# Kernel optimization log

Measured on AMD Instinct MI355X. Metric: run time of the kernel, lower is better.

The kernel has to match this reference:

```python
import jax, jax.numpy as jnp
import numpy as np

B, T, D, H, FF, TB = 4, 512, 768, 12, 3072, 64
DK = D // H
E = float(np.e)
NEG = -1e9  # stand-in for float('-inf') masked_fill; rows always have valid entries


def layer_norm(x, g, b, eps=1e-5):
    m = jnp.mean(x, axis=-1, keepdims=True)
    v = jnp.mean((x - m) ** 2, axis=-1, keepdims=True)
    return (x - m) * jax.lax.rsqrt(v + eps) * g + b


def setup_inputs() -> dict:
    key = jax.random.key(0)
    ks = jax.random.split(key, 20)
    s = 0.02
    w = lambda k, shape: jax.random.normal(k, shape, jnp.float32) * s
    return {
        "x": jax.random.normal(ks[0], (B, T, D), jnp.float32),
        "batch_temporal_mat": jax.random.uniform(ks[1], (B, T, T), jnp.float32, 0.0, 100.0),
        "padding_masks": jnp.ones((B, 1, T, T), jnp.int32),
        # attention linears (stored (in,out): y = x @ W + b, equals torch x @ W_t.T + b)
        "wq": w(ks[2], (D, D)), "bq": w(ks[3], (D,)),
        "wk": w(ks[4], (D, D)), "bk": w(ks[5], (D,)),
        "wv": w(ks[6], (D, D)), "bv": w(ks[7], (D,)),
        "wp": w(ks[8], (D, D)), "bp": w(ks[9], (D,)),
        # temporal-bias MLP: Linear(1,TB) -> leaky_relu(0.2) -> Linear(TB,1)
        "tb1_w": w(ks[10], (1, TB)), "tb1_b": w(ks[11], (TB,)),
        "tb2_w": w(ks[12], (TB, 1)), "tb2_b": w(ks[13], (1,)),
        # FFN
        "fc1_w": w(ks[14], (D, FF)), "fc1_b": w(ks[15], (FF,)),
        "fc2_w": w(ks[16], (FF, D)), "fc2_b": w(ks[17], (D,)),
        # layernorms
        "ln1_g": jnp.ones((D,), jnp.float32), "ln1_b": jnp.zeros((D,), jnp.float32),
        "ln2_g": jnp.ones((D,), jnp.float32), "ln2_b": jnp.zeros((D,), jnp.float32),
    }


def _block(x, batch_temporal_mat, padding_masks,
           wq, bq, wk, bk, wv, bv, wp, bp,
           tb1_w, tb1_b, tb2_w, tb2_b,
           fc1_w, fc1_b, fc2_w, fc2_b,
           ln1_g, ln1_b, ln2_g, ln2_b):
    # pre-LN attention sublayer
    h = layer_norm(x, ln1_g, ln1_b)
    q = (h @ wq + bq).reshape(B, T, H, DK).transpose(0, 2, 1, 3)  # (B,H,T,DK)
    k = (h @ wk + bk).reshape(B, T, H, DK).transpose(0, 2, 1, 3)
    v = (h @ wv + bv).reshape(B, T, H, DK).transpose(0, 2, 1, 3)
    scores = jnp.einsum('bhid,bhjd->bhij', q, k) * (DK ** -0.5)  # (B,H,T,T)

    # temporal bias: 1/log(e + dt), then per-(i,j) MLP with leaky_relu(0.2)
    tm = 1.0 / jnp.log(E + batch_temporal_mat)                    # (B,T,T)
    hb = jax.nn.leaky_relu(tm[..., None] @ tb1_w + tb1_b, 0.2)    # (B,T,T,TB)
    bias = (hb @ tb2_w + tb2_b)[..., 0]                           # (B,T,T)
    scores = scores + bias[:, None]

    # padding mask then causal (future) mask with CLS row 0 fully visible
    scores = jnp.where(padding_masks == 0, NEG, scores)
    causal = jnp.triu(jnp.ones((T, T), bool), 1).at[0, :].set(False)
    scores = jnp.where(causal, NEG, scores)

    p = jax.nn.softmax(scores, axis=-1)
    out = jnp.einsum('bhij,bhjd->bhid', p, v).transpose(0, 2, 1, 3).reshape(B, T, D)
    out = out @ wp + bp
    x = x + out

    # pre-LN FFN sublayer (exact GELU as in nn.GELU default)
    h2 = layer_norm(x, ln2_g, ln2_b)
    m = jax.nn.gelu(h2 @ fc1_w + fc1_b, approximate=False) @ fc2_w + fc2_b
    return x + m


def reference(x, batch_temporal_mat, padding_masks,
              wq, bq, wk, bk, wv, bv, wp, bp,
              tb1_w, tb1_b, tb2_w, tb2_b,
              fc1_w, fc1_b, fc2_w, fc2_b,
              ln1_g, ln1_b, ln2_g, ln2_b):
    return _block(x, batch_temporal_mat, padding_masks,
                  wq, bq, wk, bk, wv, bv, wp, bp,
                  tb1_w, tb1_b, tb2_w, tb2_b,
                  fc1_w, fc1_b, fc2_w, fc2_b,
                  ln1_g, ln1_b, ln2_g, ln2_b)
```

## Files before the change

### kernel.cpp

```cpp
#include <hip/hip_runtime.h>
#include <hip/hip_bf16.h>
#include <math.h>

#define B_ 4
#define T_ 512
#define D_ 768
#define H_ 12
#define FF_ 3072
#define DK_ 64
#define NTOK (B_*T_)
#define NEGV -1e9f

typedef unsigned short u16;
typedef __bf16 bfx8 __attribute__((ext_vector_type(8)));
typedef float f32x4 __attribute__((ext_vector_type(4)));
typedef u16 u16x8 __attribute__((ext_vector_type(8)));

__device__ __forceinline__ u16 f2bf(float f) {
  union { float f; unsigned u; } v; v.f = f;
  unsigned r = (v.u + 0x7FFFu + ((v.u >> 16) & 1u)) >> 16;
  return (u16)r;
}

__device__ __forceinline__ void glds16(const u16* g, u16* l) {
  __builtin_amdgcn_global_load_lds((const __attribute__((address_space(1))) void*)g,
                                   (__attribute__((address_space(3))) void*)l, 16, 0, 0);
}

__global__ __launch_bounds__(256) void prep_kernel(
    const float* __restrict__ x,
    const float* __restrict__ wq, const float* __restrict__ wk,
    const float* __restrict__ wv, const float* __restrict__ wp,
    const float* __restrict__ fc1, const float* __restrict__ fc2,
    u16* wqT, u16* wkT, u16* wvT, u16* wpT, u16* fc1T, u16* fc2T,
    const float* __restrict__ ln1g, const float* __restrict__ ln1b, u16* __restrict__ hbuf,
    const float* __restrict__ bp, float* __restrict__ x1,
    const float* __restrict__ tmat, const int* __restrict__ pad,
    const float* __restrict__ tb1w, const float* __restrict__ tb1b,
    const float* __restrict__ tb2w, const float* __restrict__ tb2b,
    float* __restrict__ biasM)
{
  const int bid = blockIdx.x;
  const int tid = threadIdx.x;
  if (bid < 6912) {
    __shared__ float tile[32][33];
    const float* in; u16* outp; int K, N, local;
    if (bid < 2304) {
      int m = bid / 576; local = bid % 576; K = 768; N = 768;
      in   = m == 0 ? wq  : (m == 1 ? wk  : (m == 2 ? wv  : wp));
      outp = m == 0 ? wqT : (m == 1 ? wkT : (m == 2 ? wvT : wpT));
    } else if (bid < 4608) {
      local = bid - 2304; K = 768; N = 3072; in = fc1; outp = fc1T;
    } else {
      local = bid - 4608; K = 3072; N = 768; in = fc2; outp = fc2T;
    }
    const int nt = N / 32;
    const int n0 = (local % nt) * 32, k0 = (local / nt) * 32;
    const int tx = tid & 31, ty = tid >> 5;
    #pragma unroll
    for (int i = 0; i < 4; ++i) {
      int r = ty + i * 8;
      tile[r][tx] = in[(size_t)(k0 + r) * N + n0 + tx];
    }
    __syncthreads();
    #pragma unroll
    for (int i = 0; i < 4; ++i) {
      int r = ty + i * 8;
      outp[(size_t)(n0 + r) * K + k0 + tx] = f2bf(tile[tx][r]);
    }
  } else if (bid < 8960) {
    const int row = bid - 6912;
    const float* xr = x + (size_t)row * D_;
    float v0 = xr[tid], v1 = xr[tid + 256], v2 = xr[tid + 512];
    float s = v0 + v1 + v2;
    float sq = v0 * v0 + v1 * v1 + v2 * v2;
    #pragma unroll
    for (int o = 32; o > 0; o >>= 1) { s += __shfl_down(s, o); sq += __shfl_down(sq, o); }
    __shared__ float ss[4], s2[4];
    int w = tid >> 6;
    if ((tid & 63) == 0) { ss[w] = s; s2[w] = sq; }
    __syncthreads();
    s = ss[0] + ss[1] + ss[2] + ss[3];
    sq = s2[0] + s2[1] + s2[2] + s2[3];
    float mean = s * (1.0f / 768.0f);
    float inv = rsqrtf(sq * (1.0f / 768.0f) - mean * mean + 1e-5f);
    u16* orow = hbuf + (size_t)row * D_;
    float* x1r = x1 + (size_t)row * D_;
    orow[tid]       = f2bf((v0 - mean) * inv * ln1g[tid]       + ln1b[tid]);
    orow[tid + 256] = f2bf((v1 - mean) * inv * ln1g[tid + 256] + ln1b[tid + 256]);
    orow[tid + 512] = f2bf((v2 - mean) * inv * ln1g[tid + 512] + ln1b[tid + 512]);
    x1r[tid]       = v0 + bp[tid];
    x1r[tid + 256] = v1 + bp[tid + 256];
    x1r[tid + 512] = v2 + bp[tid + 512];
  } else {
    __shared__ float sw1[64], sb1[64], sw2[64];
    if (tid < 64) {
      sw1[tid] = tb1w[tid];
      sb1[tid] = tb1b[tid];
      sw2[tid] = tb2w[tid];
    }
    __syncthreads();
    size_t idx = (size_t)(bid - 8960) * 256 + tid;
    float tm = 1.0f / __logf(2.718281828459045f + tmat[idx]);
    float acc = tb2b[0];
    #pragma unroll
    for (int t = 0; t < 64; ++t) {
      float u = fmaf(tm, sw1[t], sb1[t]);
      u = u > 0.0f ? u : 0.2f * u;
      acc = fmaf(u, sw2[t], acc);
    }
    biasM[idx] = (pad[idx] == 0) ? NEGV : acc;
  }
}

__device__ __forceinline__ void gemm_tile_p2(
    const u16* __restrict__ A, const u16* __restrict__ BT,
    int K, int nk, int m0, int n0, int k0,
    u16* As, u16* Bs, f32x4 acc[4][4])
{
  const int tid = threadIdx.x;
  const int w = tid >> 6, lane = tid & 63;
  const int lr = lane & 15, lk = (lane >> 4) * 8;
  const int wm = (w >> 1) * 64, wn = (w & 1) * 64;
  const int c0 = w * 64 + lane, c1 = 256 + c0;
  const int r0 = c0 >> 2, o0 = (c0 & 3) * 8;
  const int r1 = c1 >> 2, o1 = (c1 & 3) * 8;
  const u16* gA0 = A  + (size_t)(m0 + r0) * K + k0 + o0;
  const u16* gA1 = A  + (size_t)(m0 + r1) * K + k0 + o1;
  const u16* gB0 = BT + (size_t)(n0 + r0) * K + k0 + o0;
  const u16* gB1 = BT + (size_t)(n0 + r1) * K + k0 + o1;
  u16* la0 = As + w * 512;
  u16* la1 = As + 2048 + w * 512;
  u16* lb0 = Bs + w * 512;
  u16* lb1 = Bs + 2048 + w * 512;
#define ISSUE_TILE(kk, b) do { \
    glds16(gA0 + (size_t)(kk) * 32, la0 + (b) * 4096); \
    glds16(gA1 + (size_t)(kk) * 32, la1 + (b) * 4096); \
    glds16(gB0 + (size_t)(kk) * 32, lb0 + (b) * 4096); \
    glds16(gB1 + (size_t)(kk) * 32, lb1 + (b) * 4096); } while (0)
  ISSUE_TILE(0, 0);
  if (nk > 1) ISSUE_TILE(1, 1);
  int cb = 0;
  for (int kt = 0; kt < nk; ++kt) {
    if (kt < nk - 2) asm volatile("s_waitcnt vmcnt(4)" ::: "memory");
    else             asm volatile("s_waitcnt vmcnt(0)" ::: "memory");
    __builtin_amdgcn_sched_barrier(0);
    __builtin_amdgcn_s_barrier();
    __builtin_amdgcn_sched_barrier(0);
    const u16* Asc = As + cb * 4096;
    const u16* Bsc = Bs + cb * 4096;
    bfx8 af[4], bfr[4];
    #pragma unroll
    for (int t = 0; t < 4; ++t) {
      af[t]  = *(const bfx8*)&Asc[(wm + t * 16 + lr) * 32 + lk];
      bfr[t] = *(const bfx8*)&Bsc[(wn + t * 16 + lr) * 32 + lk];
    }
    #pragma unroll
    for (int rt = 0; rt < 4; ++rt)
      #pragma unroll
      for (int ct = 0; ct < 4; ++ct)
        acc[rt][ct] = __builtin_amdgcn_mfma_f32_16x16x32_bf16(af[rt], bfr[ct], acc[rt][ct], 0, 0, 0);
    if (kt + 2 < nk) {
      int nb = cb + 2; if (nb >= 3) nb -= 3;
      ISSUE_TILE(kt + 2, nb);
    }
    cb = cb + 1; if (cb >= 3) cb = 0;
  }
#undef ISSUE_TILE
}

__global__ __launch_bounds__(256) void gemm_qkv(
    const u16* __restrict__ A,
    const u16* __restrict__ wqT, const u16* __restrict__ wkT, const u16* __restrict__ wvT,
    const float* __restrict__ bq, const float* __restrict__ bk, const float* __restrict__ bv,
    u16* __restrict__ qo, u16* __restrict__ ko, u16* __restrict__ vo)
{
  __shared__ u16 As[3 * 128 * 32];
  __shared__ u16 Bs[3 * 128 * 32];
  const int z = blockIdx.z;
  const u16* BT = z == 0 ? wqT : (z == 1 ? wkT : wvT);
  const float* bias = z == 0 ? bq : (z == 1 ? bk : bv);
  u16* outp = z == 0 ? qo : (z == 1 ? ko : vo);
  const float scale = z == 0 ? 0.125f : 1.0f;
  const int m0 = blockIdx.y * 128, n0 = blockIdx.x * 128;
  f32x4 acc[4][4];
  #pragma unroll
  for (int a = 0; a < 4; ++a)
    #pragma unroll
    for (int bb = 0; bb < 4; ++bb) acc[a][bb] = (f32x4){0.f, 0.f, 0.f, 0.f};
  gemm_tile_p2(A, BT, D_, D_ / 32, m0, n0, 0, As, Bs, acc);
  const int tid = threadIdx.x;
  const int w = tid >> 6, lane = tid & 63;
  const int lr = lane & 15;
  const int wm = (w >> 1) * 64, wn = (w & 1) * 64;
  #pragma unroll
  for (int rt = 0; rt < 4; ++rt)
    #pragma unroll
    for (int ct = 0; ct < 4; ++ct)
      #pragma unroll
      for (int r = 0; r < 4; ++r) {
        int m = m0 + wm + rt * 16 + (lane >> 4) * 4 + r;
        int n = n0 + wn + ct * 16 + lr;
        float val = (acc[rt][ct][r] + bias[n]) * scale;
        int b = m >> 9, t = m & 511, hh = n >> 6, d = n & 63;
        if (z < 2) outp[(((size_t)b * H_ + hh) * T_ + t) * DK_ + d] = f2bf(val);
        else       outp[(((size_t)b * H_ + hh) * DK_ + d) * T_ + t] = f2bf(val);
      }
}

__global__ __launch_bounds__(256) void gemm_atomic(
    const u16* __restrict__ A, const u16* __restrict__ BT,
    float* __restrict__ dst, int M, int N, int K, int Ksplit)
{
  __shared__ u16 As[3 * 128 * 32];
  __shared__ u16 Bs[3 * 128 * 32];
  const int m0 = blockIdx.y * 128, n0 = blockIdx.x * 128;
  const int kz = blockIdx.z;
  f32x4 acc[4][4];
  #pragma unroll
  for (int a = 0; a < 4; ++a)
    #pragma unroll
    for (int bb = 0; bb < 4; ++bb) acc[a][bb] = (f32x4){0.f, 0.f, 0.f, 0.f};
  gemm_tile_p2(A, BT, K, Ksplit / 32, m0, n0, kz * Ksplit, As, Bs, acc);
  const int tid = threadIdx.x;
  const int w = tid >> 6, lane = tid & 63;
  const int lr = lane & 15;
  const int wm = (w >> 1) * 64, wn = (w & 1) * 64;
  #pragma unroll
  for (int rt = 0; rt < 4; ++rt)
    #pragma unroll
    for (int ct = 0; ct < 4; ++ct)
      #pragma unroll
      for (int r = 0; r < 4; ++r) {
        int m = m0 + wm + rt * 16 + (lane >> 4) * 4 + r;
        int n = n0 + wn + ct * 16 + lr;
        atomicAdd(&dst[(size_t)m * N + n], acc[rt][ct][r]);
      }
}

__global__ __launch_bounds__(256) void gemm_gelu(
    const u16* __restrict__ A, const u16* __restrict__ BT,
    const float* __restrict__ bias, u16* __restrict__ outp, int M, int N, int K)
{
  __shared__ u16 As[3 * 128 * 32];
  __shared__ u16 Bs[3 * 128 * 32];
  const int m0 = blockIdx.y * 128, n0 = blockIdx.x * 128;
  f32x4 acc[4][4];
  #pragma unroll
  for (int a = 0; a < 4; ++a)
    #pragma unroll
    for (int bb = 0; bb < 4; ++bb) acc[a][bb] = (f32x4){0.f, 0.f, 0.f, 0.f};
  gemm_tile_p2(A, BT, K, K / 32, m0, n0, 0, As, Bs, acc);
  const int tid = threadIdx.x;
  const int w = tid >> 6, lane = tid & 63;
  const int lr = lane & 15;
  const int wm = (w >> 1) * 64, wn = (w & 1) * 64;
  #pragma unroll
  for (int rt = 0; rt < 4; ++rt)
    #pragma unroll
    for (int ct = 0; ct < 4; ++ct)
      #pragma unroll
      for (int r = 0; r < 4; ++r) {
        int m = m0 + wm + rt * 16 + (lane >> 4) * 4 + r;
        int n = n0 + wn + ct * 16 + lr;
        float val = acc[rt][ct][r] + bias[n];
        float gl = 0.5f * val * (1.0f + erff(val * 0.7071067811865475f));
        outp[(size_t)m * N + n] = f2bf(gl);
      }
}

__global__ __launch_bounds__(256) void ln2_kernel(
    const float* __restrict__ x1, const float* __restrict__ g, const float* __restrict__ bta,
    const float* __restrict__ fc2b, u16* __restrict__ h2, float* __restrict__ outInit)
{
  const int row = blockIdx.x;
  const int tid = threadIdx.x;
  const size_t base = (size_t)row * D_;
  float v[3];
  float s = 0.f, sq = 0.f;
  #pragma unroll
  for (int i = 0; i < 3; ++i) {
    int c = tid + i * 256;
    float val = x1[base + c];
    v[i] = val;
    s += val; sq += val * val;
  }
  #pragma unroll
  for (int o = 32; o > 0; o >>= 1) { s += __shfl_down(s, o); sq += __shfl_down(sq, o); }
  __shared__ float ss[4], s2[4];
  int w = tid >> 6;
  if ((tid & 63) == 0) { ss[w] = s; s2[w] = sq; }
  __syncthreads();
  s = ss[0] + ss[1] + ss[2] + ss[3];
  sq = s2[0] + s2[1] + s2[2] + s2[3];
  float mean = s * (1.0f / 768.0f);
  float inv = rsqrtf(sq * (1.0f / 768.0f) - mean * mean + 1e-5f);
  #pragma unroll
  for (int i = 0; i < 3; ++i) {
    int c = tid + i * 256;
    h2[base + c] = f2bf((v[i] - mean) * inv * g[c] + bta[c]);
    outInit[base + c] = v[i] + fc2b[c];
  }
}

__global__ __launch_bounds__(256) void attn_kernel(
    const u16* __restrict__ q, const u16* __restrict__ k, const u16* __restrict__ vT,
    const float* __restrict__ biasM, u16* __restrict__ ao)
{
  __shared__ u16 P[32 * 512];
  __shared__ float pmax[128], psum[128];
  const int tid = threadIdx.x;
  const int w = tid >> 6, lane = tid & 63;
  const int lr = lane & 15, hi = lane >> 4, lk = hi * 8;

  const int bid = blockIdx.x;
  const int xcd = bid & 7, idx = bid >> 3;
  const int bh = xcd * 6 + (idx >> 4);
  const int i0 = (idx & 15) * 32;
  const int b = bh / H_, h = bh % H_;
  const int tmax = (i0 == 0) ? 31 : ((i0 >> 4) + 1);
  const int nks  = (i0 == 0) ? 16 : ((i0 >> 5) + 1);

  bfx8 qf[2][2];
  #pragma unroll
  for (int g = 0; g < 2; ++g)
    #pragma unroll
    for (int ks = 0; ks < 2; ++ks)
      qf[g][ks] = *(const bfx8*)(q + ((size_t)bh * T_ + i0 + g * 16 + lr) * DK_ + ks * 32 + lk);
  f32x4 acc[8][2];
  float mx[2][4];
  #pragma unroll
  for (int g = 0; g < 2; ++g)
    #pragma unroll
    for (int r = 0; r < 4; ++r) mx[g][r] = -3.4e38f;
  #pragma unroll
  for (int ct = 0; ct < 8; ++ct) {
    const int t = ct * 4 + w;
    if (t > tmax) continue;
    const int j0 = t * 16;
    bfx8 kf0 = *(const bfx8*)(k + ((size_t)bh * T_ + j0 + lr) * DK_ + lk);
    bfx8 kf1 = *(const bfx8*)(k + ((size_t)bh * T_ + j0 + lr) * DK_ + 32 + lk);
    const int j = j0 + lr;
    #pragma unroll
    for (int g = 0; g < 2; ++g) {
      f32x4 a0 = (f32x4){0.f, 0.f, 0.f, 0.f};
      a0 = __builtin_amdgcn_mfma_f32_16x16x32_bf16(qf[g][0], kf0, a0, 0, 0, 0);
      a0 = __builtin_amdgcn_mfma_f32_16x16x32_bf16(qf[g][1], kf1, a0, 0, 0, 0);
      #pragma unroll
      for (int r = 0; r < 4; ++r) {
        int i = i0 + g * 16 + hi * 4 + r;
        float s = a0[r] + biasM[((size_t)b * T_ + i) * T_ + j];
        if (j > i && i != 0) s = NEGV;
        a0[r] = s;
        mx[g][r] = fmaxf(mx[g][r], s);
      }
      acc[ct][g] = a0;
    }
  }
  #pragma unroll
  for (int o = 1; o < 16; o <<= 1)
    #pragma unroll
    for (int g = 0; g < 2; ++g)
      #pragma unroll
      for (int r = 0; r < 4; ++r) mx[g][r] = fmaxf(mx[g][r], __shfl_xor(mx[g][r], o));
  if (lr == 0) {
    #pragma unroll
    for (int g = 0; g < 2; ++g)
      #pragma unroll
      for (int r = 0; r < 4; ++r) pmax[w * 32 + g * 16 + hi * 4 + r] = mx[g][r];
  }
  __syncthreads();

  float M2[2][4], sm[2][4];
  #pragma unroll
  for (int g = 0; g < 2; ++g)
    #pragma unroll
    for (int r = 0; r < 4; ++r) {
      int row = g * 16 + hi * 4 + r;
      M2[g][r] = fmaxf(fmaxf(pmax[row], pmax[32 + row]), fmaxf(pmax[64 + row], pmax[96 + row]));
      sm[g][r] = 0.f;
    }
  char* Pb = (char*)P;
  #pragma unroll
  for (int ct = 0; ct < 8; ++ct) {
    const int t = ct * 4 + w;
    if (t > tmax) continue;
    const int col = t * 16 + lr;
    #pragma unroll
    for (int g = 0; g < 2; ++g)
      #pragma unroll
      for (int r = 0; r < 4; ++r) {
        float pexp = __expf(acc[ct][g][r] - M2[g][r]);
        sm[g][r] += pexp;
        int row = g * 16 + hi * 4 + r;
        int byte = (row * 1024 + col * 2) ^ ((row & 7) << 4);
        *(u16*)(Pb + byte) = f2bf(pexp);
      }
  }
  #pragma unroll
  for (int o = 1; o < 16; o <<= 1)
    #pragma unroll
    for (int g = 0; g < 2; ++g)
      #pragma unroll
      for (int r = 0; r < 4; ++r) sm[g][r] += __shfl_xor(sm[g][r], o);
  if (lr == 0) {
    #pragma unroll
    for (int g = 0; g < 2; ++g)
      #pragma unroll
      for (int r = 0; r < 4; ++r) psum[w * 32 + g * 16 + hi * 4 + r] = sm[g][r];
  }
  __syncthreads();

  float rinv[2][4];
  #pragma unroll
  for (int g = 0; g < 2; ++g)
    #pragma unroll
    for (int r = 0; r < 4; ++r) {
      int row = g * 16 + hi * 4 + r;
      rinv[g][r] = 1.0f / (psum[row] + psum[32 + row] + psum[64 + row] + psum[96 + row]);
    }

  {
    const int n0 = w * 16;
    f32x4 oa0 = (f32x4){0.f, 0.f, 0.f, 0.f};
    f32x4 oa1 = (f32x4){0.f, 0.f, 0.f, 0.f};
    for (int ks = 0; ks < nks; ++ks) {
      bfx8 vf = *(const bfx8*)(vT + ((size_t)bh * DK_ + n0 + lr) * T_ + ks * 32 + lk);
      int byte0 = (lr * 1024 + (ks * 32 + lk) * 2) ^ ((lr & 7) << 4);
      int byte1 = ((16 + lr) * 1024 + (ks * 32 + lk) * 2) ^ ((lr & 7) << 4);
      bfx8 pa0 = *(const bfx8*)(Pb + byte0);
      bfx8 pa1 = *(const bfx8*)(Pb + byte1);
      oa0 = __builtin_amdgcn_mfma_f32_16x16x32_bf16(pa0, vf, oa0, 0, 0, 0);
      oa1 = __builtin_amdgcn_mfma_f32_16x16x32_bf16(pa1, vf, oa1, 0, 0, 0);
    }
    #pragma unroll
    for (int r = 0; r < 4; ++r) {
      int i = i0 + hi * 4 + r;
      ao[((size_t)b * T_ + i) * D_ + h * DK_ + n0 + lr] = f2bf(oa0[r] * rinv[0][r]);
    }
    #pragma unroll
    for (int r = 0; r < 4; ++r) {
      int i = i0 + 16 + hi * 4 + r;
      ao[((size_t)b * T_ + i) * D_ + h * DK_ + n0 + lr] = f2bf(oa1[r] * rinv[1][r]);
    }
  }
}

extern "C" void kernel_launch(void* const* d_in, const int* in_sizes, int n_in,
                              void* d_out, int out_size, void* d_ws, size_t ws_size,
                              hipStream_t stream) {
  (void)in_sizes; (void)n_in; (void)out_size; (void)ws_size;
  const float* x    = (const float*)d_in[0];
  const float* tmat = (const float*)d_in[1];
  const int*   pad  = (const int*)d_in[2];
  const float* wq = (const float*)d_in[3];  const float* bq = (const float*)d_in[4];
  const float* wk = (const float*)d_in[5];  const float* bk = (const float*)d_in[6];
  const float* wv = (const float*)d_in[7];  const float* bv = (const float*)d_in[8];
  const float* wp = (const float*)d_in[9];  const float* bp = (const float*)d_in[10];
  const float* tb1w = (const float*)d_in[11]; const float* tb1b = (const float*)d_in[12];
  const float* tb2w = (const float*)d_in[13]; const float* tb2b = (const float*)d_in[14];
  const float* fc1w = (const float*)d_in[15]; const float* fc1b = (const float*)d_in[16];
  const float* fc2w = (const float*)d_in[17]; const float* fc2b = (const float*)d_in[18];
  const float* ln1g = (const float*)d_in[19]; const float* ln1b = (const float*)d_in[20];
  const float* ln2g = (const float*)d_in[21]; const float* ln2b = (const float*)d_in[22];
  float* out = (float*)d_out;

  char* p = (char*)d_ws;
  u16* wqT  = (u16*)p; p += (size_t)768 * 768 * 2;
  u16* wkT  = (u16*)p; p += (size_t)768 * 768 * 2;
  u16* wvT  = (u16*)p; p += (size_t)768 * 768 * 2;
  u16* wpT  = (u16*)p; p += (size_t)768 * 768 * 2;
  u16* fc1T = (u16*)p; p += (size_t)768 * 3072 * 2;
  u16* fc2T = (u16*)p; p += (size_t)3072 * 768 * 2;
  float* x1 = (float*)p; p += (size_t)NTOK * D_ * 4;
  u16* gbuf = (u16*)p; p += (size_t)NTOK * FF_ * 2;
  u16* hbuf = (u16*)p; p += (size_t)NTOK * D_ * 2;
  u16* qb   = (u16*)p; p += (size_t)NTOK * D_ * 2;
  u16* kb   = (u16*)p; p += (size_t)NTOK * D_ * 2;
  u16* vTb  = (u16*)p; p += (size_t)NTOK * D_ * 2;
  float* biasM = (float*)p; p += (size_t)B_ * T_ * T_ * 4;
  u16* ao   = (u16*)p; p += (size_t)NTOK * D_ * 2;
  u16* h2   = (u16*)p; p += (size_t)NTOK * D_ * 2;

  prep_kernel<<<13056, 256, 0, stream>>>(x, wq, wk, wv, wp, fc1w, fc2w,
                                         wqT, wkT, wvT, wpT, fc1T, fc2T,
                                         ln1g, ln1b, hbuf, bp, x1,
                                         tmat, pad, tb1w, tb1b, tb2w, tb2b, biasM);

  gemm_qkv<<<dim3(6, 16, 3), 256, 0, stream>>>(hbuf, wqT, wkT, wvT, bq, bk, bv, qb, kb, vTb);
  attn_kernel<<<768, 256, 0, stream>>>(qb, kb, vTb, biasM, ao);

  gemm_atomic<<<dim3(6, 16, 2), 256, 0, stream>>>(ao, wpT, x1, NTOK, 768, 768, 384);
  ln2_kernel<<<NTOK, 256, 0, stream>>>(x1, ln2g, ln2b, fc2b, h2, out);

  gemm_gelu<<<dim3(24, 16), 256, 0, stream>>>(h2, fc1T, fc1b, gbuf, NTOK, FF_, 768);

  gemm_atomic<<<dim3(6, 16, 4), 256, 0, stream>>>(gbuf, fc2T, out, NTOK, 768, 3072, 768);
}
```

Before: 148.5 us.

## Replace atomic split-K with bf16 partials, XCD-aware tile mapping, and MFMA prio hints

Split-K GEMMs now write bf16 partial slabs instead of float atomics. Separate reduce kernels sum the partials together with the residual and biases, so the x1 and out initialisation moves out of prep and ln2. Grid indices are remapped so neighbouring M tiles share an XCD for L2 reuse, and the next tile load is issued before the MFMAs in the GEMM loop. Attention sets s_setprio around the MFMAs and splits the score epilogue from them, and the weight transpose stores vectorised u16x4. In exchange, the bf16 partials lose precision, the workspace grows by eight slabs, and there are extra partial writes and reads.

```diff
diff --git a/kernel.cpp b/kernel.cpp
--- a/kernel.cpp
+++ b/kernel.cpp
@@ -15,11 +15,16 @@
 typedef __bf16 bfx8 __attribute__((ext_vector_type(8)));
 typedef float f32x4 __attribute__((ext_vector_type(4)));
 typedef u16 u16x8 __attribute__((ext_vector_type(8)));
+typedef u16 u16x4 __attribute__((ext_vector_type(4)));
 
 __device__ __forceinline__ u16 f2bf(float f) {
   union { float f; unsigned u; } v; v.f = f;
   unsigned r = (v.u + 0x7FFFu + ((v.u >> 16) & 1u)) >> 16;
   return (u16)r;
+}
+
+__device__ __forceinline__ float bf2f(u16 u) {
+  union { unsigned u; float f; } c; c.u = (unsigned)u << 16; return c.f;
 }
 
 __device__ __forceinline__ void glds16(const u16* g, u16* l) {
@@ -34,7 +39,6 @@
     const float* __restrict__ fc1, const float* __restrict__ fc2,
     u16* wqT, u16* wkT, u16* wvT, u16* wpT, u16* fc1T, u16* fc2T,
     const float* __restrict__ ln1g, const float* __restrict__ ln1b, u16* __restrict__ hbuf,
-    const float* __restrict__ bp, float* __restrict__ x1,
     const float* __restrict__ tmat, const int* __restrict__ pad,
     const float* __restrict__ tb1w, const float* __restrict__ tb1b,
     const float* __restrict__ tb2w, const float* __restrict__ tb2b,
@@ -63,11 +67,12 @@
       tile[r][tx] = in[(size_t)(k0 + r) * N + n0 + tx];
     }
     __syncthreads();
-    #pragma unroll
-    for (int i = 0; i < 4; ++i) {
-      int r = ty + i * 8;
-      outp[(size_t)(n0 + r) * K + k0 + tx] = f2bf(tile[tx][r]);
-    }
+    const int nloc = tid >> 3;
+    const int k4   = (tid & 7) * 4;
+    u16x4 vv;
+    #pragma unroll
+    for (int jj = 0; jj < 4; ++jj) vv[jj] = f2bf(tile[k4 + jj][nloc]);
+    *(u16x4*)&outp[(size_t)(n0 + nloc) * K + k0 + k4] = vv;
   } else if (bid < 8960) {
     const int row = bid - 6912;
     const float* xr = x + (size_t)row * D_;
@@ -85,13 +90,9 @@
     float mean = s * (1.0f / 768.0f);
     float inv = rsqrtf(sq * (1.0f / 768.0f) - mean * mean + 1e-5f);
     u16* orow = hbuf + (size_t)row * D_;
-    float* x1r = x1 + (size_t)row * D_;
     orow[tid]       = f2bf((v0 - mean) * inv * ln1g[tid]       + ln1b[tid]);
     orow[tid + 256] = f2bf((v1 - mean) * inv * ln1g[tid + 256] + ln1b[tid + 256]);
     orow[tid + 512] = f2bf((v2 - mean) * inv * ln1g[tid + 512] + ln1b[tid + 512]);
-    x1r[tid]       = v0 + bp[tid];
-    x1r[tid + 256] = v1 + bp[tid + 256];
-    x1r[tid + 512] = v2 + bp[tid + 512];
   } else {
     __shared__ float sw1[64], sb1[64], sw2[64];
     if (tid < 64) {
@@ -155,15 +156,15 @@
       af[t]  = *(const bfx8*)&Asc[(wm + t * 16 + lr) * 32 + lk];
       bfr[t] = *(const bfx8*)&Bsc[(wn + t * 16 + lr) * 32 + lk];
     }
-    #pragma unroll
-    for (int rt = 0; rt < 4; ++rt)
-      #pragma unroll
-      for (int ct = 0; ct < 4; ++ct)
-        acc[rt][ct] = __builtin_amdgcn_mfma_f32_16x16x32_bf16(af[rt], bfr[ct], acc[rt][ct], 0, 0, 0);
     if (kt + 2 < nk) {
       int nb = cb + 2; if (nb >= 3) nb -= 3;
       ISSUE_TILE(kt + 2, nb);
     }
+    #pragma unroll
+    for (int rt = 0; rt < 4; ++rt)
+      #pragma unroll
+      for (int ct = 0; ct < 4; ++ct)
+        acc[rt][ct] = __builtin_amdgcn_mfma_f32_16x16x32_bf16(af[rt], bfr[ct], acc[rt][ct], 0, 0, 0);
     cb = cb + 1; if (cb >= 3) cb = 0;
   }
 #undef ISSUE_TILE
@@ -177,12 +178,16 @@
 {
   __shared__ u16 As[3 * 128 * 32];
   __shared__ u16 Bs[3 * 128 * 32];
-  const int z = blockIdx.z;
+  const int bid = blockIdx.x;
+  const int xcd = bid & 7, idx = bid >> 3;
+  const int y = xcd * 2 + (idx & 1);
+  const int r2 = idx >> 1;
+  const int xt = r2 % 6, z = r2 / 6;
   const u16* BT = z == 0 ? wqT : (z == 1 ? wkT : wvT);
   const float* bias = z == 0 ? bq : (z == 1 ? bk : bv);
   u16* outp = z == 0 ? qo : (z == 1 ? ko : vo);
   const float scale = z == 0 ? 0.125f : 1.0f;
-  const int m0 = blockIdx.y * 128, n0 = blockIdx.x * 128;
+  const int m0 = y * 128, n0 = xt * 128;
   f32x4 acc[4][4];
   #pragma unroll
   for (int a = 0; a < 4; ++a)
@@ -208,14 +213,18 @@
       }
 }
 
-__global__ __launch_bounds__(256) void gemm_atomic(
+__global__ __launch_bounds__(256) void gemm_part_bf16(
     const u16* __restrict__ A, const u16* __restrict__ BT,
-    float* __restrict__ dst, int M, int N, int K, int Ksplit)
+    u16* __restrict__ part, int M, int N, int K, int Ksplit, int nx)
 {
   __shared__ u16 As[3 * 128 * 32];
   __shared__ u16 Bs[3 * 128 * 32];
-  const int m0 = blockIdx.y * 128, n0 = blockIdx.x * 128;
-  const int kz = blockIdx.z;
+  const int bid = blockIdx.x;
+  const int xcd = bid & 7, idx = bid >> 3;
+  const int y = xcd * 2 + (idx & 1);
+  const int r2 = idx >> 1;
+  const int xt = r2 % nx, kz = r2 / nx;
+  const int m0 = y * 128, n0 = xt * 128;
   f32x4 acc[4][4];
   #pragma unroll
   for (int a = 0; a < 4; ++a)
@@ -226,6 +235,7 @@
   const int w = tid >> 6, lane = tid & 63;
   const int lr = lane & 15;
   const int wm = (w >> 1) * 64, wn = (w & 1) * 64;
+  u16* pp = part + (size_t)kz * M * N;
   #pragma unroll
   for (int rt = 0; rt < 4; ++rt)
     #pragma unroll
@@ -234,54 +244,27 @@
       for (int r = 0; r < 4; ++r) {
         int m = m0 + wm + rt * 16 + (lane >> 4) * 4 + r;
         int n = n0 + wn + ct * 16 + lr;
-        atomicAdd(&dst[(size_t)m * N + n], acc[rt][ct][r]);
+        pp[(size_t)m * N + n] = f2bf(acc[rt][ct][r]);
       }
 }
 
-__global__ __launch_bounds__(256) void gemm_gelu(
-    const u16* __restrict__ A, const u16* __restrict__ BT,
-    const float* __restrict__ bias, u16* __restrict__ outp, int M, int N, int K)
-{
-  __shared__ u16 As[3 * 128 * 32];
-  __shared__ u16 Bs[3 * 128 * 32];
-  const int m0 = blockIdx.y * 128, n0 = blockIdx.x * 128;
-  f32x4 acc[4][4];
-  #pragma unroll
-  for (int a = 0; a < 4; ++a)
-    #pragma unroll
-    for (int bb = 0; bb < 4; ++bb) acc[a][bb] = (f32x4){0.f, 0.f, 0.f, 0.f};
-  gemm_tile_p2(A, BT, K, K / 32, m0, n0, 0, As, Bs, acc);
-  const int tid = threadIdx.x;
-  const int w = tid >> 6, lane = tid & 63;
-  const int lr = lane & 15;
-  const int wm = (w >> 1) * 64, wn = (w & 1) * 64;
-  #pragma unroll
-  for (int rt = 0; rt < 4; ++rt)
-    #pragma unroll
-    for (int ct = 0; ct < 4; ++ct)
-      #pragma unroll
-      for (int r = 0; r < 4; ++r) {
-        int m = m0 + wm + rt * 16 + (lane >> 4) * 4 + r;
-        int n = n0 + wn + ct * 16 + lr;
-        float val = acc[rt][ct][r] + bias[n];
-        float gl = 0.5f * val * (1.0f + erff(val * 0.7071067811865475f));
-        outp[(size_t)m * N + n] = f2bf(gl);
-      }
-}
-
-__global__ __launch_bounds__(256) void ln2_kernel(
-    const float* __restrict__ x1, const float* __restrict__ g, const float* __restrict__ bta,
-    const float* __restrict__ fc2b, u16* __restrict__ h2, float* __restrict__ outInit)
+__global__ __launch_bounds__(256) void reduce_ln(
+    const u16* __restrict__ part, const float* __restrict__ x, const float* __restrict__ bp,
+    const float* __restrict__ g, const float* __restrict__ bta,
+    float* __restrict__ x1, u16* __restrict__ h2)
 {
   const int row = blockIdx.x;
   const int tid = threadIdx.x;
   const size_t base = (size_t)row * D_;
+  const size_t slab = (size_t)NTOK * D_;
   float v[3];
   float s = 0.f, sq = 0.f;
   #pragma unroll
   for (int i = 0; i < 3; ++i) {
     int c = tid + i * 256;
-    float val = x1[base + c];
+    float val = x[base + c] + bp[c];
+    #pragma unroll
+    for (int kz = 0; kz < 4; ++kz) val += bf2f(part[kz * slab + base + c]);
     v[i] = val;
     s += val; sq += val * val;
   }
@@ -298,9 +281,70 @@
   #pragma unroll
   for (int i = 0; i < 3; ++i) {
     int c = tid + i * 256;
+    x1[base + c] = v[i];
     h2[base + c] = f2bf((v[i] - mean) * inv * g[c] + bta[c]);
-    outInit[base + c] = v[i] + fc2b[c];
-  }
+  }
+}
+
+__global__ __launch_bounds__(256) void reduce_out(
+    const u16* __restrict__ part, const float* __restrict__ x1,
+    const float* __restrict__ bias, float* __restrict__ out)
+{
+  const size_t base = ((size_t)blockIdx.x * 256 + threadIdx.x) * 8;
+  const size_t slab = (size_t)NTOK * D_;
+  const int nb = (int)(base % D_);
+  float s[8];
+  float4 a0 = *(const float4*)&x1[base];
+  float4 a1 = *(const float4*)&x1[base + 4];
+  float4 b0 = *(const float4*)&bias[nb];
+  float4 b1 = *(const float4*)&bias[nb + 4];
+  s[0] = a0.x + b0.x; s[1] = a0.y + b0.y; s[2] = a0.z + b0.z; s[3] = a0.w + b0.w;
+  s[4] = a1.x + b1.x; s[5] = a1.y + b1.y; s[6] = a1.z + b1.z; s[7] = a1.w + b1.w;
+  #pragma unroll
+  for (int kz = 0; kz < 8; ++kz) {
+    u16x8 pv = *(const u16x8*)&part[kz * slab + base];
+    #pragma unroll
+    for (int j = 0; j < 8; ++j) s[j] += bf2f(pv[j]);
+  }
+  float4 o0 = {s[0], s[1], s[2], s[3]};
+  float4 o1 = {s[4], s[5], s[6], s[7]};
+  *(float4*)&out[base]     = o0;
+  *(float4*)&out[base + 4] = o1;
+}
+
+__global__ __launch_bounds__(256) void gemm_gelu(
+    const u16* __restrict__ A, const u16* __restrict__ BT,
+    const float* __restrict__ bias, u16* __restrict__ outp, int M, int N, int K)
+{
+  __shared__ u16 As[3 * 128 * 32];
+  __shared__ u16 Bs[3 * 128 * 32];
+  const int bid = blockIdx.x;
+  const int xcd = bid & 7, idx = bid >> 3;
+  const int y = xcd * 2 + (idx & 1);
+  const int xt = idx >> 1;
+  const int m0 = y * 128, n0 = xt * 128;
+  f32x4 acc[4][4];
+  #pragma unroll
+  for (int a = 0; a < 4; ++a)
+    #pragma unroll
+    for (int bb = 0; bb < 4; ++bb) acc[a][bb] = (f32x4){0.f, 0.f, 0.f, 0.f};
+  gemm_tile_p2(A, BT, K, K / 32, m0, n0, 0, As, Bs, acc);
+  const int tid = threadIdx.x;
+  const int w = tid >> 6, lane = tid & 63;
+  const int lr = lane & 15;
+  const int wm = (w >> 1) * 64, wn = (w & 1) * 64;
+  #pragma unroll
+  for (int rt = 0; rt < 4; ++rt)
+    #pragma unroll
+    for (int ct = 0; ct < 4; ++ct)
+      #pragma unroll
+      for (int r = 0; r < 4; ++r) {
+        int m = m0 + wm + rt * 16 + (lane >> 4) * 4 + r;
+        int n = n0 + wn + ct * 16 + lr;
+        float val = acc[rt][ct][r] + bias[n];
+        float gl = 0.5f * val * (1.0f + erff(val * 0.7071067811865475f));
+        outp[(size_t)m * N + n] = f2bf(gl);
+      }
 }
 
 __global__ __launch_bounds__(256) void attn_kernel(
@@ -341,21 +385,25 @@
     bfx8 kf0 = *(const bfx8*)(k + ((size_t)bh * T_ + j0 + lr) * DK_ + lk);
     bfx8 kf1 = *(const bfx8*)(k + ((size_t)bh * T_ + j0 + lr) * DK_ + 32 + lk);
     const int j = j0 + lr;
+    __builtin_amdgcn_s_setprio(1);
     #pragma unroll
     for (int g = 0; g < 2; ++g) {
       f32x4 a0 = (f32x4){0.f, 0.f, 0.f, 0.f};
       a0 = __builtin_amdgcn_mfma_f32_16x16x32_bf16(qf[g][0], kf0, a0, 0, 0, 0);
       a0 = __builtin_amdgcn_mfma_f32_16x16x32_bf16(qf[g][1], kf1, a0, 0, 0, 0);
+      acc[ct][g] = a0;
+    }
+    __builtin_amdgcn_s_setprio(0);
+    #pragma unroll
+    for (int g = 0; g < 2; ++g)
       #pragma unroll
       for (int r = 0; r < 4; ++r) {
         int i = i0 + g * 16 + hi * 4 + r;
-        float s = a0[r] + biasM[((size_t)b * T_ + i) * T_ + j];
+        float s = acc[ct][g][r] + biasM[((size_t)b * T_ + i) * T_ + j];
         if (j > i && i != 0) s = NEGV;
-        a0[r] = s;
+        acc[ct][g][r] = s;
         mx[g][r] = fmaxf(mx[g][r], s);
       }
-      acc[ct][g] = a0;
-    }
   }
   #pragma unroll
   for (int o = 1; o < 16; o <<= 1)
@@ -430,8 +478,10 @@
       int byte1 = ((16 + lr) * 1024 + (ks * 32 + lk) * 2) ^ ((lr & 7) << 4);
       bfx8 pa0 = *(const bfx8*)(Pb + byte0);
       bfx8 pa1 = *(const bfx8*)(Pb + byte1);
+      __builtin_amdgcn_s_setprio(1);
       oa0 = __builtin_amdgcn_mfma_f32_16x16x32_bf16(pa0, vf, oa0, 0, 0, 0);
       oa1 = __builtin_amdgcn_mfma_f32_16x16x32_bf16(pa1, vf, oa1, 0, 0, 0);
+      __builtin_amdgcn_s_setprio(0);
     }
     #pragma unroll
     for (int r = 0; r < 4; ++r) {
@@ -481,19 +531,21 @@
   float* biasM = (float*)p; p += (size_t)B_ * T_ * T_ * 4;
   u16* ao   = (u16*)p; p += (size_t)NTOK * D_ * 2;
   u16* h2   = (u16*)p; p += (size_t)NTOK * D_ * 2;
+  u16* partF = (u16*)p; p += (size_t)8 * NTOK * D_ * 2;
 
   prep_kernel<<<13056, 256, 0, stream>>>(x, wq, wk, wv, wp, fc1w, fc2w,
                                          wqT, wkT, wvT, wpT, fc1T, fc2T,
-                                         ln1g, ln1b, hbuf, bp, x1,
+                                         ln1g, ln1b, hbuf,
                                          tmat, pad, tb1w, tb1b, tb2w, tb2b, biasM);
 
-  gemm_qkv<<<dim3(6, 16, 3), 256, 0, stream>>>(hbuf, wqT, wkT, wvT, bq, bk, bv, qb, kb, vTb);
+  gemm_qkv<<<288, 256, 0, stream>>>(hbuf, wqT, wkT, wvT, bq, bk, bv, qb, kb, vTb);
   attn_kernel<<<768, 256, 0, stream>>>(qb, kb, vTb, biasM, ao);
 
-  gemm_atomic<<<dim3(6, 16, 2), 256, 0, stream>>>(ao, wpT, x1, NTOK, 768, 768, 384);
-  ln2_kernel<<<NTOK, 256, 0, stream>>>(x1, ln2g, ln2b, fc2b, h2, out);
-
-  gemm_gelu<<<dim3(24, 16), 256, 0, stream>>>(h2, fc1T, fc1b, gbuf, NTOK, FF_, 768);
-
-  gemm_atomic<<<dim3(6, 16, 4), 256, 0, stream>>>(gbuf, fc2T, out, NTOK, 768, 3072, 768);
-}
+  gemm_part_bf16<<<384, 256, 0, stream>>>(ao, wpT, partF, NTOK, 768, 768, 192, 6);
+  reduce_ln<<<NTOK, 256, 0, stream>>>(partF, x, bp, ln2g, ln2b, x1, h2);
+
+  gemm_gelu<<<384, 256, 0, stream>>>(h2, fc1T, fc1b, gbuf, NTOK, FF_, 768);
+
+  gemm_part_bf16<<<768, 256, 0, stream>>>(gbuf, fc2T, partF, NTOK, 768, 3072, 384, 6);
+  reduce_out<<<NTOK * D_ / 8 / 256, 256, 0, stream>>>(partF, x1, fc2b, out);
+}
```

Result: faster. 127.1 us (-14.4%).
